# Kernel tuning notes

Measured on AMD Instinct MI355X. Metric: run time of the kernel, lower is better.

## Reference

```python
import jax, jax.numpy as jnp
import numpy as np

KH = KW = 3
K = KH * KW
PAD = 1


def conv3x3(x, w, b):
    # x: [B,C,H,W], w: [O,C,3,3], b: [O]
    y = jax.lax.conv_general_dilated(x, w, (1, 1), ((PAD, PAD), (PAD, PAD)),
                                     dimension_numbers=('NCHW', 'OIHW', 'NCHW'))
    return y + b[None, :, None, None]


def deform_conv(x, offsets, w, b):
    # torchvision DeformConv2d, stride=1, pad=1, dilation=1, groups=1, offset_groups=1
    # x: [B,C,H,W], offsets: [B,2*K,H,W] ordered (dy,dx) per kernel point, w: [O,C,3,3]
    B, C, H, W = x.shape
    O = w.shape[0]
    off = offsets.reshape(B, K, 2, H, W)
    dy, dx = off[:, :, 0], off[:, :, 1]                      # [B,K,H,W]
    kyy, kxx = jnp.meshgrid(jnp.arange(KH), jnp.arange(KW), indexing='ij')
    ky = kyy.reshape(K).astype(x.dtype)
    kx = kxx.reshape(K).astype(x.dtype)
    py = dy + ky[None, :, None, None] + jnp.arange(H, dtype=x.dtype)[None, None, :, None] - PAD
    px = dx + kx[None, :, None, None] + jnp.arange(W, dtype=x.dtype)[None, None, None, :] - PAD
    y0 = jnp.floor(py)
    x0 = jnp.floor(px)
    wy = (py - y0)[:, None]                                   # [B,1,K,H,W]
    wx = (px - x0)[:, None]
    y0i = y0.astype(jnp.int32)
    x0i = x0.astype(jnp.int32)
    xf = x.reshape(B, C, H * W)

    def gather(yi, xi):
        valid = (yi >= 0) & (yi < H) & (xi >= 0) & (xi < W)   # zero outside
        yc = jnp.clip(yi, 0, H - 1)
        xc = jnp.clip(xi, 0, W - 1)
        idx = (yc * W + xc).reshape(B, 1, K * H * W)
        g = jnp.take_along_axis(xf, idx, axis=2).reshape(B, C, K, H, W)
        return g * valid[:, None].astype(x.dtype)

    v00 = gather(y0i, x0i)
    v01 = gather(y0i, x0i + 1)
    v10 = gather(y0i + 1, x0i)
    v11 = gather(y0i + 1, x0i + 1)
    samp = (v00 * (1 - wy) * (1 - wx) + v01 * (1 - wy) * wx
            + v10 * wy * (1 - wx) + v11 * wy * wx)            # [B,C,K,H,W]
    out = jnp.einsum('bckhw,ock->bohw', samp, w.reshape(O, C, K))
    return out + b[None, :, None, None]


def deform_align(x, y, wo, bo, wd, bd):
    return deform_conv(x, conv3x3(y, wo, bo), wd, bd)


def setup_inputs() -> dict:
    key = jax.random.key(0)
    ks = jax.random.split(key, 16)
    inC, embedC = 64, 96
    B, H, W = 4, 96, 96
    s = 0.02
    d = {
        'x1': jax.random.normal(ks[0], (B, inC, H, W), jnp.float32),
        'y': jax.random.normal(ks[1], (B, inC, H, W), jnp.float32),
        # block 1: offset conv inC->2K, deform conv inC->embedC
        'wo1': jax.random.normal(ks[2], (2 * K, inC, 3, 3), jnp.float32) * s,
        'bo1': jnp.zeros((2 * K,), jnp.float32),
        'wd1': jax.random.normal(ks[3], (embedC, inC, 3, 3), jnp.float32) * s,
        'bd1': jnp.zeros((embedC,), jnp.float32),
        # block 2: embedC->2K, embedC->embedC
        'wo2': jax.random.normal(ks[4], (2 * K, embedC, 3, 3), jnp.float32) * s,
        'bo2': jnp.zeros((2 * K,), jnp.float32),
        'wd2': jax.random.normal(ks[5], (embedC, embedC, 3, 3), jnp.float32) * s,
        'bd2': jnp.zeros((embedC,), jnp.float32),
        # block 3: embedC->2K, embedC->inC
        'wo3': jax.random.normal(ks[6], (2 * K, embedC, 3, 3), jnp.float32) * s,
        'bo3': jnp.zeros((2 * K,), jnp.float32),
        'wd3': jax.random.normal(ks[7], (inC, embedC, 3, 3), jnp.float32) * s,
        'bd3': jnp.zeros((inC,), jnp.float32),
    }
    return d


def reference(x1, y, wo1, bo1, wd1, bd1, wo2, bo2, wd2, bd2, wo3, bo3, wd3, bd3):
    h = deform_align(x1, y, wo1, bo1, wd1, bd1)
    h = deform_align(h, h, wo2, bo2, wd2, bd2)
    h = deform_align(h, h, wo3, bo3, wd3, bd3)
    return h
```

## Files before the change

### kernel.cpp

```cpp
#include <hip/hip_runtime.h>

constexpr int B = 4, H = 96, W = 96, HW = H * W;
constexpr int NPIX = B * HW;
constexpr int KOFF = 18;

typedef _Float16 half8 __attribute__((ext_vector_type(8)));
typedef _Float16 half4 __attribute__((ext_vector_type(4)));
typedef float f32x4 __attribute__((ext_vector_type(4)));

__device__ __forceinline__ int iclamp(int v, int lo, int hi) {
  return v < lo ? lo : (v > hi ? hi : v);
}

struct Corners {
  int i00, i01, i10, i11;
  float w00, w01, w10, w11;
};

__device__ __forceinline__ Corners mk_corners(float py, float qx) {
  float fy = floorf(py), fx = floorf(qx);
  float wy = py - fy, wx = qx - fx;
  int y0 = (int)fy, x0 = (int)fx;
  int y1 = y0 + 1, x1 = x0 + 1;
  bool vy0 = (y0 >= 0) & (y0 < H);
  bool vy1 = (y1 >= 0) & (y1 < H);
  bool vx0 = (x0 >= 0) & (x0 < W);
  bool vx1 = (x1 >= 0) & (x1 < W);
  int r0 = iclamp(y0, 0, H - 1) * W;
  int r1 = iclamp(y1, 0, H - 1) * W;
  int c0 = iclamp(x0, 0, W - 1);
  int c1 = iclamp(x1, 0, W - 1);
  Corners cc;
  cc.i00 = r0 + c0; cc.i01 = r0 + c1; cc.i10 = r1 + c0; cc.i11 = r1 + c1;
  float a = 1.f - wy, bb = 1.f - wx;
  cc.w00 = a * bb * ((vy0 & vx0) ? 1.f : 0.f);
  cc.w01 = a * wx * ((vy0 & vx1) ? 1.f : 0.f);
  cc.w10 = wy * bb * ((vy1 & vx0) ? 1.f : 0.f);
  cc.w11 = wy * wx * ((vy1 & vx1) ? 1.f : 0.f);
  return cc;
}

template <int KS>
__device__ __forceinline__ void load_corners(const _Float16* xb, int ch, const Corners& cc,
                                             half8 r[KS][4]) {
  const _Float16* p00 = xb + (size_t)cc.i00 * (KS * 32) + ch;
  const _Float16* p01 = xb + (size_t)cc.i01 * (KS * 32) + ch;
  const _Float16* p10 = xb + (size_t)cc.i10 * (KS * 32) + ch;
  const _Float16* p11 = xb + (size_t)cc.i11 * (KS * 32) + ch;
#pragma unroll
  for (int ks = 0; ks < KS; ++ks) {
    r[ks][0] = *(const half8*)(p00 + ks * 32);
    r[ks][1] = *(const half8*)(p01 + ks * 32);
    r[ks][2] = *(const half8*)(p10 + ks * 32);
    r[ks][3] = *(const half8*)(p11 + ks * 32);
  }
}

template <int KS>
__device__ __forceinline__ void interp_corners(const Corners& cc, half8 r[KS][4],
                                               half8 a[KS]) {
  _Float16 q00 = (_Float16)cc.w00, q01 = (_Float16)cc.w01;
  _Float16 q10 = (_Float16)cc.w10, q11 = (_Float16)cc.w11;
#pragma unroll
  for (int ks = 0; ks < KS; ++ks)
    a[ks] = r[ks][0] * q00 + r[ks][1] * q01 + r[ks][2] * q10 + r[ks][3] * q11;
}

template <int KS>
__device__ __forceinline__ void load_shift(const _Float16* xb, int ch, int h, int w,
                                           int ky, int kx, half8 a[KS]) {
  int yy = h + ky, xx = w + kx;
  bool v = (yy >= 0) & (yy < H) & (xx >= 0) & (xx < W);
  const _Float16* pv = xb + (size_t)(yy * W + xx) * (KS * 32) + ch;
#pragma unroll
  for (int ks = 0; ks < KS; ++ks) {
    half8 r = {0, 0, 0, 0, 0, 0, 0, 0};
    if (v) r = *(const half8*)(pv + ks * 32);
    a[ks] = r;
  }
}

template <int KS, int NJ>
__device__ __forceinline__ void mfma_tap1(const _Float16* wk, int lane,
                                          half8 a[KS], f32x4 acc[NJ]) {
#pragma unroll
  for (int ks = 0; ks < KS; ++ks)
#pragma unroll
    for (int j = 0; j < NJ; ++j) {
      half8 b = *(const half8*)(wk + ((size_t)(ks * NJ + j) * 64 + lane) * 8);
      acc[j] = __builtin_amdgcn_mfma_f32_16x16x32_f16(a[ks], b, acc[j], 0, 0, 0);
    }
}

struct WAll {
  const float* src[6];
  _Float16* dst[6];
  int C[6], Osrc[6], OPAD[6], base[6];
};

__global__ void wfrag_all_kernel(WAll wa) {
  int bid = blockIdx.x;
  int s = 0;
#pragma unroll
  for (int i = 1; i < 6; ++i) s += (bid >= wa.base[i]) ? 1 : 0;
  int fid = bid - wa.base[s];
  int C = wa.C[s], Osrc = wa.Osrc[s], OPAD = wa.OPAD[s];
  const float* wsrc = wa.src[s];
  _Float16* wf = wa.dst[s];
  int KS = C / 32;
  int NJ = OPAD / 16;
  int lane = threadIdx.x;
  int j = fid % NJ;
  int ks = (fid / NJ) % KS;
  int k = fid / (NJ * KS);
  int o = j * 16 + (lane & 15);
  int c0 = ks * 32 + (lane >> 4) * 8;
  half8 v;
#pragma unroll
  for (int u = 0; u < 8; ++u)
    v[u] = (o < Osrc) ? (_Float16)wsrc[((size_t)o * C + c0 + u) * 9 + k] : (_Float16)0.f;
  *(half8*)(wf + ((size_t)fid * 64 + lane) * 8) = v;
}

__global__ __launch_bounds__(256) void repack2_kernel(const float* __restrict__ in0,
                                                      const float* __restrict__ in1,
                                                      _Float16* __restrict__ o0,
                                                      _Float16* __restrict__ o1) {
  constexpr int C = 64;
  const float* in = blockIdx.y ? in1 : in0;
  _Float16* outh = blockIdx.y ? o1 : o0;
  __shared__ float tile[64 * C];
  int t = threadIdx.x;
  int pix0 = blockIdx.x * 64;
  int b = pix0 / HW;
  int hw0 = pix0 - b * HW;
  int l = t & 63;
  for (int cc = t >> 6; cc < C; cc += 4)
    tile[cc * 64 + l] = in[((size_t)b * C + cc) * HW + hw0 + l];
  __syncthreads();
  int pl = t >> 2;
  int cq = t & 3;
  _Float16* op = outh + (size_t)(pix0 + pl) * C + cq * (C / 4);
#pragma unroll
  for (int c = 0; c < C / 4; c += 4) {
    half4 hv;
#pragma unroll
    for (int u = 0; u < 4; ++u) hv[u] = (_Float16)tile[(cq * (C / 4) + c + u) * 64 + pl];
    *(half4*)(op + c) = hv;
  }
}

template <int C, int O, bool WF32, bool WH>
__global__ __launch_bounds__(64, 2)
void stage_kernel(const _Float16* __restrict__ xoff, const _Float16* __restrict__ xdef,
                  const _Float16* __restrict__ wfo, const float* __restrict__ bo,
                  const _Float16* __restrict__ wfd, const float* __restrict__ bd,
                  float* __restrict__ out, _Float16* __restrict__ outh) {
  constexpr int KS = C / 32;
  constexpr int NJ = O / 16;
  const int lane = threadIdx.x;
  const int row = lane & 15;
  const int kgrp = lane >> 4;
  const int ch = kgrp * 8;
  const int px0 = blockIdx.x * 16;
  const int b = px0 / HW;
  const int hw0 = px0 - b * HW;
  const int hwm = hw0 + row;
  const int h0 = hwm / W, w0 = hwm - h0 * W;
  const _Float16* xo = xoff + (size_t)b * HW * C;
  const _Float16* xd = xdef + (size_t)b * HW * C;

  __shared__ float lofs[16][KOFF];

  {
    f32x4 aoc[2];
#pragma unroll
    for (int j = 0; j < 2; ++j) {
      int o = j * 16 + row;
      float bv = (o < KOFF) ? bo[o] : 0.f;
      aoc[j] = {bv, bv, bv, bv};
    }
    half8 a[KS];
    load_shift<KS>(xo, ch, h0, w0, -1, -1, a);
#pragma unroll
    for (int k = 0; k < 9; ++k) {
      const _Float16* wk = wfo + (size_t)k * (KS * 2 * 512);
      if (k < 8) {
        int kn = k + 1;
        half8 n[KS];
        load_shift<KS>(xo, ch, h0, w0, kn / 3 - 1, kn % 3 - 1, n);
        mfma_tap1<KS, 2>(wk, lane, a, aoc);
#pragma unroll
        for (int ks = 0; ks < KS; ++ks) a[ks] = n[ks];
      } else {
        mfma_tap1<KS, 2>(wk, lane, a, aoc);
      }
    }
#pragma unroll
    for (int j = 0; j < 2; ++j) {
      int o = j * 16 + row;
      if (o < KOFF) {
#pragma unroll
        for (int r = 0; r < 4; ++r) lofs[kgrp * 4 + r][o] = aoc[j][r];
      }
    }
  }
  __syncthreads();

  float2 of[9];
#pragma unroll
  for (int k = 0; k < 9; ++k) of[k] = {lofs[row][2 * k], lofs[row][2 * k + 1]};
  const float hf = (float)(h0 - 1), wwf = (float)(w0 - 1);

  f32x4 acc[NJ];
#pragma unroll
  for (int j = 0; j < NJ; ++j) {
    float bv = bd[j * 16 + row];
    acc[j] = {bv, bv, bv, bv};
  }
  half8 a[KS];
  {
    Corners cA = mk_corners(of[0].x + hf, of[0].y + wwf);
    half8 r0[KS][4];
    load_corners<KS>(xd, ch, cA, r0);
    interp_corners<KS>(cA, r0, a);
  }
#pragma unroll
  for (int k = 0; k < 9; ++k) {
    const _Float16* wk = wfd + (size_t)k * (KS * NJ * 512);
    if (k < 8) {
      int kn = k + 1;
      float kyf = (float)(kn / 3), kxf = (float)(kn % 3);
      Corners cA = mk_corners(of[kn].x + hf + kyf, of[kn].y + wwf + kxf);
      half8 r0[KS][4];
      load_corners<KS>(xd, ch, cA, r0);
      mfma_tap1<KS, NJ>(wk, lane, a, acc);
      interp_corners<KS>(cA, r0, a);
    } else {
      mfma_tap1<KS, NJ>(wk, lane, a, acc);
    }
  }
#pragma unroll
  for (int j = 0; j < NJ; ++j) {
    int o = j * 16 + row;
#pragma unroll
    for (int r = 0; r < 4; ++r) {
      int p = px0 + kgrp * 4 + r;
      if (WF32) out[((size_t)b * O + o) * HW + (p - b * HW)] = acc[j][r];
      if (WH) outh[(size_t)p * O + o] = (_Float16)acc[j][r];
    }
  }
}

extern "C" void kernel_launch(void* const* d_in, const int* in_sizes, int n_in,
                              void* d_out, int out_size, void* d_ws, size_t ws_size,
                              hipStream_t stream) {
  const float* x1  = (const float*)d_in[0];
  const float* y   = (const float*)d_in[1];
  const float* wo1 = (const float*)d_in[2];
  const float* bo1 = (const float*)d_in[3];
  const float* wd1 = (const float*)d_in[4];
  const float* bd1 = (const float*)d_in[5];
  const float* wo2 = (const float*)d_in[6];
  const float* bo2 = (const float*)d_in[7];
  const float* wd2 = (const float*)d_in[8];
  const float* bd2 = (const float*)d_in[9];
  const float* wo3 = (const float*)d_in[10];
  const float* bo3 = (const float*)d_in[11];
  const float* wd3 = (const float*)d_in[12];
  const float* bd3 = (const float*)d_in[13];
  float* out = (float*)d_out;

  char* p = (char*)d_ws;
  auto alloc = [&](size_t bytes) {
    char* r = p;
    p += (bytes + 255) & ~(size_t)255;
    return r;
  };
  _Float16* Wo1f = (_Float16*)alloc((size_t)9 * 2 * 2 * 512 * 2);
  _Float16* Wo2f = (_Float16*)alloc((size_t)9 * 3 * 2 * 512 * 2);
  _Float16* Wo3f = (_Float16*)alloc((size_t)9 * 3 * 2 * 512 * 2);
  _Float16* W1f  = (_Float16*)alloc((size_t)9 * 2 * 6 * 512 * 2);
  _Float16* W2f  = (_Float16*)alloc((size_t)9 * 3 * 6 * 512 * 2);
  _Float16* W3f  = (_Float16*)alloc((size_t)9 * 3 * 4 * 512 * 2);
  _Float16* x1h = (_Float16*)alloc((size_t)NPIX * 64 * 2);
  _Float16* yh  = (_Float16*)alloc((size_t)NPIX * 64 * 2);
  _Float16* h1h = (_Float16*)alloc((size_t)NPIX * 96 * 2);
  _Float16* h2h = (_Float16*)alloc((size_t)NPIX * 96 * 2);

  WAll wa;
  wa.src[0] = wo1; wa.dst[0] = Wo1f; wa.C[0] = 64; wa.Osrc[0] = 18; wa.OPAD[0] = 32;
  wa.src[1] = wo2; wa.dst[1] = Wo2f; wa.C[1] = 96; wa.Osrc[1] = 18; wa.OPAD[1] = 32;
  wa.src[2] = wo3; wa.dst[2] = Wo3f; wa.C[2] = 96; wa.Osrc[2] = 18; wa.OPAD[2] = 32;
  wa.src[3] = wd1; wa.dst[3] = W1f;  wa.C[3] = 64; wa.Osrc[3] = 96; wa.OPAD[3] = 96;
  wa.src[4] = wd2; wa.dst[4] = W2f;  wa.C[4] = 96; wa.Osrc[4] = 96; wa.OPAD[4] = 96;
  wa.src[5] = wd3; wa.dst[5] = W3f;  wa.C[5] = 96; wa.Osrc[5] = 64; wa.OPAD[5] = 64;
  int base = 0;
  for (int i = 0; i < 6; ++i) {
    wa.base[i] = base;
    base += 9 * (wa.C[i] / 32) * (wa.OPAD[i] / 16);
  }
  hipLaunchKernelGGL(wfrag_all_kernel, dim3(base), dim3(64), 0, stream, wa);
  hipLaunchKernelGGL(repack2_kernel, dim3(NPIX / 64, 2), dim3(256), 0, stream,
                     x1, y, x1h, yh);

  dim3 gs(NPIX / 16);
  dim3 wb(64);

  hipLaunchKernelGGL((stage_kernel<64, 96, false, true>), gs, wb, 0, stream,
                     yh, x1h, Wo1f, bo1, W1f, bd1, (float*)nullptr, h1h);
  hipLaunchKernelGGL((stage_kernel<96, 96, false, true>), gs, wb, 0, stream,
                     h1h, h1h, Wo2f, bo2, W2f, bd2, (float*)nullptr, h2h);
  hipLaunchKernelGGL((stage_kernel<96, 64, true, false>), gs, wb, 0, stream,
                     h2h, h2h, Wo3f, bo3, W3f, bd3, out, (_Float16*)nullptr);
}
```

Baseline: 131.2 us.

## Split output channels across two waves per block and swizzle blocks for XCD locality

Each block now runs two waves over the same 16 pixels, and each wave computes half of the output-channel fragments, so per-wave accumulator registers shrink and occupancy can rise. Both waves redundantly compute the offset convolution and the bilinear corner gathers and interpolation into per-wave shared slots, which lets the block-wide barrier be removed. Block indices are remapped so consecutive chunks land on the same XCD, aimed at better L2 reuse of neighbouring pixels. The cost is duplicated gather and interpolation work plus offset-conv MFMAs in every wave.

```diff
diff --git a/kernel.cpp b/kernel.cpp
--- a/kernel.cpp
+++ b/kernel.cpp
@@ -80,14 +80,14 @@
   }
 }
 
-template <int KS, int NJ>
-__device__ __forceinline__ void mfma_tap1(const _Float16* wk, int lane,
-                                          half8 a[KS], f32x4 acc[NJ]) {
+template <int KS, int NJ, int NJW>
+__device__ __forceinline__ void mfma_tap1(const _Float16* wk, int lane, int jbase,
+                                          half8 a[KS], f32x4 acc[NJW]) {
 #pragma unroll
   for (int ks = 0; ks < KS; ++ks)
 #pragma unroll
-    for (int j = 0; j < NJ; ++j) {
-      half8 b = *(const half8*)(wk + ((size_t)(ks * NJ + j) * 64 + lane) * 8);
+    for (int j = 0; j < NJW; ++j) {
+      half8 b = *(const half8*)(wk + ((size_t)(ks * NJ + jbase + j) * 64 + lane) * 8);
       acc[j] = __builtin_amdgcn_mfma_f32_16x16x32_f16(a[ks], b, acc[j], 0, 0, 0);
     }
 }
@@ -151,18 +151,22 @@
 }
 
 template <int C, int O, bool WF32, bool WH>
-__global__ __launch_bounds__(64, 2)
+__global__ __launch_bounds__(128, 4)
 void stage_kernel(const _Float16* __restrict__ xoff, const _Float16* __restrict__ xdef,
                   const _Float16* __restrict__ wfo, const float* __restrict__ bo,
                   const _Float16* __restrict__ wfd, const float* __restrict__ bd,
                   float* __restrict__ out, _Float16* __restrict__ outh) {
   constexpr int KS = C / 32;
   constexpr int NJ = O / 16;
-  const int lane = threadIdx.x;
+  constexpr int NJW = NJ / 2;
+  const int tid = threadIdx.x;
+  const int wid = tid >> 6;
+  const int lane = tid & 63;
   const int row = lane & 15;
   const int kgrp = lane >> 4;
   const int ch = kgrp * 8;
-  const int px0 = blockIdx.x * 16;
+  const int chunk = (blockIdx.x & 7) * (int)(gridDim.x >> 3) + (blockIdx.x >> 3);
+  const int px0 = chunk * 16;
   const int b = px0 / HW;
   const int hw0 = px0 - b * HW;
   const int hwm = hw0 + row;
@@ -170,7 +174,7 @@
   const _Float16* xo = xoff + (size_t)b * HW * C;
   const _Float16* xd = xdef + (size_t)b * HW * C;
 
-  __shared__ float lofs[16][KOFF];
+  __shared__ float lofs[2][16][KOFF];
 
   {
     f32x4 aoc[2];
@@ -189,11 +193,11 @@
         int kn = k + 1;
         half8 n[KS];
         load_shift<KS>(xo, ch, h0, w0, kn / 3 - 1, kn % 3 - 1, n);
-        mfma_tap1<KS, 2>(wk, lane, a, aoc);
+        mfma_tap1<KS, 2, 2>(wk, lane, 0, a, aoc);
 #pragma unroll
         for (int ks = 0; ks < KS; ++ks) a[ks] = n[ks];
       } else {
-        mfma_tap1<KS, 2>(wk, lane, a, aoc);
+        mfma_tap1<KS, 2, 2>(wk, lane, 0, a, aoc);
       }
     }
 #pragma unroll
@@ -201,21 +205,21 @@
       int o = j * 16 + row;
       if (o < KOFF) {
 #pragma unroll
-        for (int r = 0; r < 4; ++r) lofs[kgrp * 4 + r][o] = aoc[j][r];
+        for (int r = 0; r < 4; ++r) lofs[wid][kgrp * 4 + r][o] = aoc[j][r];
       }
     }
   }
-  __syncthreads();
 
   float2 of[9];
 #pragma unroll
-  for (int k = 0; k < 9; ++k) of[k] = {lofs[row][2 * k], lofs[row][2 * k + 1]};
+  for (int k = 0; k < 9; ++k) of[k] = {lofs[wid][row][2 * k], lofs[wid][row][2 * k + 1]};
   const float hf = (float)(h0 - 1), wwf = (float)(w0 - 1);
-
-  f32x4 acc[NJ];
-#pragma unroll
-  for (int j = 0; j < NJ; ++j) {
-    float bv = bd[j * 16 + row];
+  const int jbase = wid * NJW;
+
+  f32x4 acc[NJW];
+#pragma unroll
+  for (int j = 0; j < NJW; ++j) {
+    float bv = bd[(jbase + j) * 16 + row];
     acc[j] = {bv, bv, bv, bv};
   }
   half8 a[KS];
@@ -234,15 +238,15 @@
       Corners cA = mk_corners(of[kn].x + hf + kyf, of[kn].y + wwf + kxf);
       half8 r0[KS][4];
       load_corners<KS>(xd, ch, cA, r0);
-      mfma_tap1<KS, NJ>(wk, lane, a, acc);
+      mfma_tap1<KS, NJ, NJW>(wk, lane, jbase, a, acc);
       interp_corners<KS>(cA, r0, a);
     } else {
-      mfma_tap1<KS, NJ>(wk, lane, a, acc);
-    }
-  }
-#pragma unroll
-  for (int j = 0; j < NJ; ++j) {
-    int o = j * 16 + row;
+      mfma_tap1<KS, NJ, NJW>(wk, lane, jbase, a, acc);
+    }
+  }
+#pragma unroll
+  for (int j = 0; j < NJW; ++j) {
+    int o = (jbase + j) * 16 + row;
 #pragma unroll
     for (int r = 0; r < 4; ++r) {
       int p = px0 + kgrp * 4 + r;
@@ -305,7 +309,7 @@
                      x1, y, x1h, yh);
 
   dim3 gs(NPIX / 16);
-  dim3 wb(64);
+  dim3 wb(128);
 
   hipLaunchKernelGGL((stage_kernel<64, 96, false, true>), gs, wb, 0, stream,
                      yh, x1h, Wo1f, bo1, W1f, bd1, (float*)nullptr, h1h);
```

After: 193.0 us. 1.47x slower.
